# Optimization experiments

Measured on AMD Instinct MI355X. Metric: run time of the kernel, lower is better.

The kernel has to match this reference:

```python
import jax, jax.numpy as jnp
import numpy as np

SIGMA = 2.0


def _level(h, centers, W, b):
    # h: [n_prev, d], centers: [n_cur, d], W: [d, d] (torch Linear weight), b: [d]
    # squared distances via expansion: ||h||^2 - 2 h.c + ||c||^2  -> [n_prev, n_cur]
    sq = (jnp.sum(h * h, axis=1, keepdims=True)
          - 2.0 * (h @ centers.T)
          + jnp.sum(centers * centers, axis=1)[None, :])
    p = jax.nn.softmax(-sq / (2.0 * SIGMA), axis=1)  # softmax over centers per row
    t = jnp.tanh(h @ W.T + b)                        # [n_prev, d]
    # h_next[i] = sum_j p[j, i] * t[j]
    return p.T @ t                                   # [n_cur, d]


def setup_inputs() -> dict:
    key = jax.random.key(0)
    ks = jax.random.split(key, 11)
    d = 1024
    num_centers = [16384, 2048, 256, 32]
    inp = {"task_embedding": jax.random.normal(ks[0], (num_centers[0], d), dtype=jnp.float32)}
    # cluster centers per level (torch.rand -> uniform [0,1))
    inp["centers1"] = jax.random.uniform(ks[1], (num_centers[1], d), dtype=jnp.float32)
    inp["centers2"] = jax.random.uniform(ks[2], (num_centers[2], d), dtype=jnp.float32)
    inp["centers3"] = jax.random.uniform(ks[3], (num_centers[3], d), dtype=jnp.float32)
    # linear layers (Kaiming-uniform-ish init bound)
    bound = 1.0 / np.sqrt(d)
    for i, kw, kb in [(1, ks[4], ks[5]), (2, ks[6], ks[7]), (3, ks[8], ks[9])]:
        inp[f"W{i}"] = jax.random.uniform(kw, (d, d), minval=-bound, maxval=bound, dtype=jnp.float32)
        inp[f"b{i}"] = jax.random.uniform(kb, (d,), minval=-bound, maxval=bound, dtype=jnp.float32)
    return inp


def reference(task_embedding, centers1, centers2, centers3, W1, b1, W2, b2, W3, b3):
    h = task_embedding
    h = _level(h, centers1, W1, b1)
    h = _level(h, centers2, W2, b2)
    h = _level(h, centers3, W3, b3)
    return h
```

## Files before the change

kernel.cpp:

```cpp
#include <hip/hip_runtime.h>
#include <cmath>

typedef _Float16 half8 __attribute__((ext_vector_type(8)));
typedef _Float16 half4v __attribute__((ext_vector_type(4)));
typedef __attribute__((ext_vector_type(4))) float floatx4;

#define GLOAD_LDS16(gp, lp)                                            \
  __builtin_amdgcn_global_load_lds(                                    \
      (const __attribute__((address_space(1))) void*)(gp),             \
      (__attribute__((address_space(3))) void*)(lp), 16, 0, 0)

static inline int cdiv(int a, int b) { return (a + b - 1) / b; }

__global__ void prep(const float* __restrict__ h0, const float* __restrict__ W1,
                     const float* __restrict__ W2, const float* __restrict__ W3,
                     const float* __restrict__ c1, const float* __restrict__ c2,
                     const float* __restrict__ c3,
                     _Float16* __restrict__ hh, _Float16* __restrict__ Wh1,
                     _Float16* __restrict__ Wh2, _Float16* __restrict__ Wh3,
                     _Float16* __restrict__ cb1, _Float16* __restrict__ cb2,
                     _Float16* __restrict__ cb3,
                     float* __restrict__ cn1, float* __restrict__ cn2,
                     float* __restrict__ cn3,
                     int nh, int nw, int castBlocks, int n1, int n2) {
  int t = threadIdx.x;
  if ((int)blockIdx.x < castBlocks) {
    int gi = (blockIdx.x * 256 + t) * 4;
    const float* src; _Float16* dst; int off;
    if (gi < nh)                { src = h0; dst = hh;  off = gi; }
    else if (gi < nh + nw)      { src = W1; dst = Wh1; off = gi - nh; }
    else if (gi < nh + 2 * nw)  { src = W2; dst = Wh2; off = gi - nh - nw; }
    else if (gi < nh + 3 * nw)  { src = W3; dst = Wh3; off = gi - nh - 2 * nw; }
    else return;
    float4 v = *(const float4*)(src + off);
    half4v o = {(_Float16)v.x, (_Float16)v.y, (_Float16)v.z, (_Float16)v.w};
    *(half4v*)(dst + off) = o;
    return;
  }
  int row = blockIdx.x - castBlocks;
  const float* c; _Float16* cb; float* cn;
  if (row < n1)            { c = c1; cb = cb1; cn = cn1; }
  else if (row < n1 + n2)  { row -= n1; c = c2; cb = cb2; cn = cn2; }
  else                     { row -= n1 + n2; c = c3; cb = cb3; cn = cn3; }
  float4 v = *(const float4*)(c + (size_t)row * 1024 + t * 4);
  half4v o = {(_Float16)v.x, (_Float16)v.y, (_Float16)v.z, (_Float16)v.w};
  *(half4v*)(cb + (size_t)row * 1024 + t * 4) = o;
  float s = v.x * v.x + v.y * v.y + v.z * v.z + v.w * v.w;
  #pragma unroll
  for (int off = 32; off > 0; off >>= 1) s += __shfl_down(s, off, 64);
  __shared__ float ws[4];
  if ((t & 63) == 0) ws[t >> 6] = s;
  __syncthreads();
  if (t == 0) cn[row] = ws[0] + ws[1] + ws[2] + ws[3];
}

#define SM_CHUNK 64
__global__ void colexp_partial(_Float16* __restrict__ ST, const float* __restrict__ pmax,
                               float* __restrict__ psum, int mchunks, int ncur, int nprev) {
  int col = (blockIdx.x * 256 + threadIdx.x) * 4;
  if (col >= nprev) return;
  float m0 = -1e30f, m1 = -1e30f, m2 = -1e30f, m3 = -1e30f;
  for (int k = 0; k < mchunks; ++k) {
    float4 v = *(const float4*)(pmax + (size_t)k * nprev + col);
    m0 = fmaxf(m0, v.x); m1 = fmaxf(m1, v.y); m2 = fmaxf(m2, v.z); m3 = fmaxf(m3, v.w);
  }
  int j0 = blockIdx.y * SM_CHUNK;
  int j1 = min(j0 + SM_CHUNK, ncur);
  float s0 = 0.f, s1 = 0.f, s2 = 0.f, s3 = 0.f;
  for (int j = j0; j < j1; ++j) {
    size_t o = (size_t)j * nprev + col;
    half4v x = *(const half4v*)(ST + o);
    float e0 = __expf((float)x[0] - m0), e1 = __expf((float)x[1] - m1);
    float e2 = __expf((float)x[2] - m2), e3 = __expf((float)x[3] - m3);
    half4v e = {(_Float16)e0, (_Float16)e1, (_Float16)e2, (_Float16)e3};
    *(half4v*)(ST + o) = e;
    s0 += e0; s1 += e1; s2 += e2; s3 += e3;
  }
  float4 sv = {s0, s1, s2, s3};
  *(float4*)(psum + (size_t)blockIdx.y * nprev + col) = sv;
}

__global__ void reduce_parts(const _Float16* __restrict__ part, _Float16* __restrict__ out,
                             int mn, int S) {
  int i = (blockIdx.x * 256 + threadIdx.x) * 4;
  if (i >= mn) return;
  float a0 = 0.f, a1 = 0.f, a2 = 0.f, a3 = 0.f;
  for (int s = 0; s < S; ++s) {
    half4v v = *(const half4v*)(part + (size_t)s * mn + i);
    a0 += (float)v[0]; a1 += (float)v[1]; a2 += (float)v[2]; a3 += (float)v[3];
  }
  half4v o = {(_Float16)a0, (_Float16)a1, (_Float16)a2, (_Float16)a3};
  *(half4v*)(out + i) = o;
}

enum { EP_LOGIT = 0, EP_TANH = 1, EP_TANHP = 2, EP_F16 = 3, EP_F32 = 4, EP_PART = 5 };

template<int BM, int BN, int EPI>
__launch_bounds__(256, 4)
__global__ void gemm_nt(const _Float16* __restrict__ A,
                        const _Float16* __restrict__ B,
                        void* __restrict__ Cout,
                        const float* __restrict__ aux1,
                        const float* __restrict__ aux2,
                        float* __restrict__ pmax,
                        int pnchunks,
                        int M, int N, int K, int kLen) {
  constexpr int BK = 64;
  constexpr int WTM = BM / 2, WTN = BN / 2;
  constexpr int FM = WTM / 16, FN = WTN / 16;
  __shared__ __align__(16) _Float16 As[BM * BK];
  __shared__ __align__(16) _Float16 Bs[BN * BK];
  float* smf = (float*)As;
  const int tid  = threadIdx.x;
  const int lane = tid & 63;
  const int wave = tid >> 6;
  const int wm = wave >> 1, wn = wave & 1;
  const int mBase = blockIdx.x * BM, nBase = blockIdx.y * BN;
  const int kBase = blockIdx.z * kLen;
  const int lr    = lane & 15;
  const int kHalf = (lane >> 4) << 3;

  const int srOff  = lane >> 3;
  const int schunk = (lane & 7) ^ srOff;
  floatx4 acc[FM][FN] = {};
  constexpr int AV = BM * BK / (256 * 8);
  constexpr int BV = BN * BK / (256 * 8);

  for (int k0 = kBase; k0 < kBase + kLen; k0 += BK) {
    #pragma unroll
    for (int v = 0; v < AV; ++v) {
      int rowBase = v * 32 + wave * 8;
      int gm = mBase + rowBase + srOff;
      if (gm >= M) gm = M - 1;
      GLOAD_LDS16(A + (size_t)gm * K + k0 + schunk * 8, &As[rowBase * BK]);
    }
    #pragma unroll
    for (int v = 0; v < BV; ++v) {
      int rowBase = v * 32 + wave * 8;
      int gn = nBase + rowBase + srOff;
      if (gn >= N) gn = N - 1;
      GLOAD_LDS16(B + (size_t)gn * K + k0 + schunk * 8, &Bs[rowBase * BK]);
    }
    __syncthreads();
    #pragma unroll
    for (int kk = 0; kk < BK; kk += 32) {
      const int q = (kk + kHalf) >> 3;
      half8 af[FM], bfv[FN];
      #pragma unroll
      for (int i = 0; i < FM; ++i) {
        int r = wm * WTM + i * 16 + lr;
        af[i] = *(const half8*)(&As[r * BK + ((q ^ (r & 7)) << 3)]);
      }
      #pragma unroll
      for (int j = 0; j < FN; ++j) {
        int r = wn * WTN + j * 16 + lr;
        bfv[j] = *(const half8*)(&Bs[r * BK + ((q ^ (r & 7)) << 3)]);
      }
      #pragma unroll
      for (int i = 0; i < FM; ++i)
        #pragma unroll
        for (int j = 0; j < FN; ++j)
          acc[i][j] = __builtin_amdgcn_mfma_f32_16x16x32_f16(af[i], bfv[j], acc[i][j], 0, 0, 0);
    }
    __syncthreads();
  }

  if (EPI == EP_TANH) {
    if (tid < BN) {
      int col = nBase + tid;
      float ssum = 0.f;
      if (col < N)
        for (int k = 0; k < pnchunks; ++k) ssum += aux2[(size_t)k * N + col];
      smf[tid] = 1.f / ssum;
    }
    __syncthreads();
  }

  const int rBase = (lane >> 4) << 2;
  float lmax[FN];
  #pragma unroll
  for (int j = 0; j < FN; ++j) lmax[j] = -1e30f;
  #pragma unroll
  for (int i = 0; i < FM; ++i) {
    #pragma unroll
    for (int j = 0; j < FN; ++j) {
      #pragma unroll
      for (int r = 0; r < 4; ++r) {
        int row = mBase + wm * WTM + i * 16 + rBase + r;
        int col = nBase + wn * WTN + j * 16 + lr;
        if (row < M && col < N) {
          float v = acc[i][j][r];
          size_t o = (size_t)row * N + col;
          if (EPI == EP_LOGIT) {
            v = 0.5f * v - 0.25f * aux1[row];
            ((_Float16*)Cout)[o] = (_Float16)v;
            lmax[j] = fmaxf(lmax[j], v);
          } else if (EPI == EP_TANH) {
            v = tanhf(v + aux1[row]) * smf[col - nBase];
            ((_Float16*)Cout)[o] = (_Float16)v;
          } else if (EPI == EP_TANHP) {
            v = tanhf(v + aux1[row]);
            ((_Float16*)Cout)[o] = (_Float16)v;
          } else if (EPI == EP_F16) {
            ((_Float16*)Cout)[o] = (_Float16)v;
          } else if (EPI == EP_PART) {
            ((_Float16*)Cout)[(size_t)blockIdx.z * M * N + o] = (_Float16)v;
          } else {
            ((float*)Cout)[o] = v;
          }
        }
      }
    }
  }
  if (EPI == EP_LOGIT) {
    #pragma unroll
    for (int j = 0; j < FN; ++j) {
      float m = lmax[j];
      m = fmaxf(m, __shfl_xor(m, 16, 64));
      m = fmaxf(m, __shfl_xor(m, 32, 64));
      if ((lane >> 4) == 0) smf[wm * BN + wn * WTN + j * 16 + lr] = m;
    }
    __syncthreads();
    if (tid < BN) {
      int col = nBase + tid;
      if (col < N)
        pmax[(size_t)blockIdx.x * N + col] = fmaxf(smf[tid], smf[BN + tid]);
    }
  }
}

template<int BM, int BN>
__launch_bounds__(256, 2)
__global__ void fused_ls(const _Float16* __restrict__ A,
                         const _Float16* __restrict__ B,
                         _Float16* __restrict__ Eout,
                         const float* __restrict__ cn,
                         int M, int N, int K) {
  constexpr int BK = 64;
  constexpr int WTM = BM / 2, WTN = BN / 2;
  constexpr int FM = WTM / 16, FN = WTN / 16;
  constexpr int TLD = BN + 4;
  constexpr int STAGE_B = (BM + BN) * BK * 2;
  constexpr int TILE_B  = BM * TLD * 4;
  constexpr int SM_B = STAGE_B > TILE_B ? STAGE_B : TILE_B;
  __shared__ __align__(16) char smem[SM_B];
  _Float16* As = (_Float16*)smem;
  _Float16* Bs = As + BM * BK;
  float* tile = (float*)smem;
  __shared__ float redm[256], reds[256];
  const int tid  = threadIdx.x;
  const int lane = tid & 63;
  const int wave = tid >> 6;
  const int wm = wave >> 1, wn = wave & 1;
  const int nBase = blockIdx.x * BN;
  const int lr    = lane & 15;
  const int kHalf = (lane >> 4) << 3;
  const int srOff  = lane >> 3;
  const int schunk = (lane & 7) ^ srOff;
  floatx4 acc[FM][FN] = {};
  constexpr int AV = BM * BK / (256 * 8);
  constexpr int BV = BN * BK / (256 * 8);

  for (int k0 = 0; k0 < K; k0 += BK) {
    #pragma unroll
    for (int v = 0; v < AV; ++v) {
      int rowBase = v * 32 + wave * 8;
      GLOAD_LDS16(A + (size_t)(rowBase + srOff) * K + k0 + schunk * 8, &As[rowBase * BK]);
    }
    #pragma unroll
    for (int v = 0; v < BV; ++v) {
      int rowBase = v * 32 + wave * 8;
      GLOAD_LDS16(B + (size_t)(nBase + rowBase + srOff) * K + k0 + schunk * 8, &Bs[rowBase * BK]);
    }
    __syncthreads();
    #pragma unroll
    for (int kk = 0; kk < BK; kk += 32) {
      const int q = (kk + kHalf) >> 3;
      half8 af[FM], bfv[FN];
      #pragma unroll
      for (int i = 0; i < FM; ++i) {
        int r = wm * WTM + i * 16 + lr;
        af[i] = *(const half8*)(&As[r * BK + ((q ^ (r & 7)) << 3)]);
      }
      #pragma unroll
      for (int j = 0; j < FN; ++j) {
        int r = wn * WTN + j * 16 + lr;
        bfv[j] = *(const half8*)(&Bs[r * BK + ((q ^ (r & 7)) << 3)]);
      }
      #pragma unroll
      for (int i = 0; i < FM; ++i)
        #pragma unroll
        for (int j = 0; j < FN; ++j)
          acc[i][j] = __builtin_amdgcn_mfma_f32_16x16x32_f16(af[i], bfv[j], acc[i][j], 0, 0, 0);
    }
    __syncthreads();
  }

  const int rBase = (lane >> 4) << 2;
  #pragma unroll
  for (int i = 0; i < FM; ++i)
    #pragma unroll
    for (int j = 0; j < FN; ++j)
      #pragma unroll
      for (int r = 0; r < 4; ++r) {
        int row = wm * WTM + i * 16 + rBase + r;
        int col = wn * WTN + j * 16 + lr;
        tile[row * TLD + col] = 0.5f * acc[i][j][r] - 0.25f * cn[row];
      }
  __syncthreads();

  constexpr int P = 256 / BN;
  const int c = tid & (BN - 1);
  const int p = tid / BN;
  float m = -1e30f;
  for (int j = p; j < M; j += P) m = fmaxf(m, tile[j * TLD + c]);
  redm[p * BN + c] = m;
  __syncthreads();
  float mf = redm[c];
  #pragma unroll
  for (int q = 1; q < P; ++q) mf = fmaxf(mf, redm[q * BN + c]);
  float s = 0.f;
  for (int j = p; j < M; j += P) {
    float e = __expf(tile[j * TLD + c] - mf);
    tile[j * TLD + c] = e;
    s += e;
  }
  reds[p * BN + c] = s;
  __syncthreads();
  float l = 0.f;
  #pragma unroll
  for (int q = 0; q < P; ++q) l += reds[q * BN + c];
  const float li = 1.f / l;
  for (int j = p; j < M; j += P)
    Eout[(size_t)j * N + nBase + c] = (_Float16)(tile[j * TLD + c] * li);
}

template<int EPI>
static int launch_gemm(int M, int N, int K, const _Float16* A, const _Float16* B,
                       void* C, const float* a1, const float* a2, float* pmax,
                       int pnchunks, hipStream_t s) {
  long b128   = (long)cdiv(M, 128) * cdiv(N, 128);
  long b12864 = (long)cdiv(M, 128) * cdiv(N, 64);
  if (b128 >= 192) {
    gemm_nt<128, 128, EPI><<<dim3(cdiv(M, 128), cdiv(N, 128)), 256, 0, s>>>(
        A, B, C, a1, a2, pmax, pnchunks, M, N, K, K);
    return 128;
  } else if (M >= 128 && b12864 >= 192) {
    gemm_nt<128, 64, EPI><<<dim3(cdiv(M, 128), cdiv(N, 64)), 256, 0, s>>>(
        A, B, C, a1, a2, pmax, pnchunks, M, N, K, K);
    return 128;
  } else {
    gemm_nt<64, 64, EPI><<<dim3(cdiv(M, 64), cdiv(N, 64)), 256, 0, s>>>(
        A, B, C, a1, a2, pmax, pnchunks, M, N, K, K);
    return 64;
  }
}

static void launch_gemm_splitk(int M, int N, int K, int S,
                               const _Float16* A, const _Float16* B,
                               _Float16* Cpart, _Float16* Cout, hipStream_t s) {
  int kLen = K / S;
  long b128 = (long)cdiv(M, 128) * cdiv(N, 128) * S;
  if (M >= 128 && N >= 128 && b128 >= 256) {
    gemm_nt<128, 128, EP_PART><<<dim3(cdiv(M, 128), cdiv(N, 128), S), 256, 0, s>>>(
        A, B, Cpart, nullptr, nullptr, nullptr, 0, M, N, K, kLen);
  } else {
    gemm_nt<64, 64, EP_PART><<<dim3(cdiv(M, 64), cdiv(N, 64), S), 256, 0, s>>>(
        A, B, Cpart, nullptr, nullptr, nullptr, 0, M, N, K, kLen);
  }
  int mn = M * N;
  reduce_parts<<<cdiv(mn, 1024), 256, 0, s>>>(Cpart, Cout, mn, S);
}

extern "C" void kernel_launch(void* const* d_in, const int* in_sizes, int n_in,
                              void* d_out, int out_size, void* d_ws, size_t ws_size,
                              hipStream_t stream) {
  const float* h0 = (const float*)d_in[0];
  const float* c1 = (const float*)d_in[1];
  const float* c2 = (const float*)d_in[2];
  const float* c3 = (const float*)d_in[3];
  const float* W1 = (const float*)d_in[4];
  const float* b1 = (const float*)d_in[5];
  const float* W2 = (const float*)d_in[6];
  const float* b2 = (const float*)d_in[7];
  const float* W3 = (const float*)d_in[8];
  const float* b3 = (const float*)d_in[9];

  const int d = 1024;
  const int N0 = 16384, N1 = 2048, N2 = 256, N3 = 32;

  char* w = (char*)d_ws;
  size_t off = 0;
  auto alloc = [&](size_t bytes) {
    void* p = w + off;
    off += (bytes + 255) & ~(size_t)255;
    return p;
  };
  _Float16* hb  = (_Float16*)alloc((size_t)N0 * d * 2);
  _Float16* cb1 = (_Float16*)alloc((size_t)N1 * d * 2);
  _Float16* cb2 = (_Float16*)alloc((size_t)N2 * d * 2);
  _Float16* cb3 = (_Float16*)alloc((size_t)N3 * d * 2);
  float* cn1 = (float*)alloc((size_t)N1 * 4);
  float* cn2 = (float*)alloc((size_t)N2 * 4);
  float* cn3 = (float*)alloc((size_t)N3 * 4);
  _Float16* Wb1 = (_Float16*)alloc((size_t)d * d * 2);
  _Float16* Wb2 = (_Float16*)alloc((size_t)d * d * 2);
  _Float16* Wb3 = (_Float16*)alloc((size_t)d * d * 2);
  _Float16* ST = (_Float16*)alloc((size_t)N1 * N0 * 2);
  _Float16* tT = (_Float16*)alloc((size_t)d * N0 * 2);
  float* pmax = (float*)alloc((size_t)32 * N0 * 4);
  float* psum = (float*)alloc((size_t)32 * N0 * 4);
  _Float16* h1b = (_Float16*)alloc((size_t)N1 * d * 2);
  _Float16* h2b = (_Float16*)alloc((size_t)N2 * d * 2);
  _Float16* Cpart = (_Float16*)alloc((size_t)8 * N1 * d * 2);
  _Float16* E = ST;
  (void)ws_size; (void)in_sizes; (void)n_in; (void)out_size;

  int nh = N0 * d, nw = d * d;
  int castBlocks = cdiv(nh + 3 * nw, 1024);
  prep<<<castBlocks + N1 + N2 + N3, 256, 0, stream>>>(
      h0, W1, W2, W3, c1, c2, c3, hb, Wb1, Wb2, Wb3, cb1, cb2, cb3,
      cn1, cn2, cn3, nh, nw, castBlocks, N1, N2);

  int bm = launch_gemm<EP_LOGIT>(N1, N0, d, cb1, hb, ST, cn1, nullptr, pmax, 0, stream);
  colexp_partial<<<dim3(N0 / 1024, cdiv(N1, SM_CHUNK)), 256, 0, stream>>>(
      ST, pmax, psum, cdiv(N1, bm), N1, N0);
  launch_gemm<EP_TANH>(d, N0, d, Wb1, hb, tT, b1, psum, nullptr, cdiv(N1, SM_CHUNK), stream);
  launch_gemm_splitk(N1, d, N0, 8, E, tT, Cpart, h1b, stream);

  fused_ls<256, 64><<<N1 / 64, 256, 0, stream>>>(cb2, h1b, E, cn2, N2, N1, d);
  launch_gemm<EP_TANHP>(d, N1, d, Wb2, h1b, tT, b2, nullptr, nullptr, 0, stream);
  launch_gemm_splitk(N2, d, N1, 8, E, tT, Cpart, h2b, stream);

  fused_ls<32, 64><<<N2 / 64, 256, 0, stream>>>(cb3, h2b, E, cn3, N3, N2, d);
  launch_gemm<EP_TANHP>(d, N2, d, Wb3, h2b, tT, b3, nullptr, nullptr, 0, stream);
  launch_gemm<EP_F32>(N3, d, N2, E, tT, d_out, nullptr, nullptr, nullptr, 0, stream);
}
```

Before: 483.4 us.

## Add 256x256 8-wave pipelined MFMA GEMM for level-1 large GEMMs

```diff
diff --git a/kernel.cpp b/kernel.cpp
--- a/kernel.cpp
+++ b/kernel.cpp
@@ -227,6 +227,212 @@
         pmax[(size_t)blockIdx.x * N + col] = fmaxf(smf[tid], smf[BN + tid]);
     }
   }
+}
+
+#define BAR8 __builtin_amdgcn_s_barrier()
+#define LGKM0 asm volatile("s_waitcnt lgkmcnt(0)" ::: "memory")
+#define VMC(n) asm volatile("s_waitcnt vmcnt(" #n ")" ::: "memory")
+#define STG_A(b, kk, h)                                                              \
+  do {                                                                               \
+    GLOAD_LDS16(gA + (size_t)((h) * 128) * K + (kk),                                 \
+                &As[b][((h) * 128 + wave * 8) * 64]);                                \
+    GLOAD_LDS16(gA + (size_t)((h) * 128 + 64) * K + (kk),                            \
+                &As[b][((h) * 128 + 64 + wave * 8) * 64]);                           \
+  } while (0)
+#define STG_B(b, kk, h)                                                              \
+  do {                                                                               \
+    GLOAD_LDS16(gB + (size_t)((h) * 128) * K + (kk),                                 \
+                &Bs[b][((h) * 128 + wave * 8) * 64]);                                \
+    GLOAD_LDS16(gB + (size_t)((h) * 128 + 64) * K + (kk),                            \
+                &Bs[b][((h) * 128 + 64 + wave * 8) * 64]);                           \
+  } while (0)
+#define LDA8(s, base)                                                                \
+  { _Pragma("unroll") for (int i_ = 0; i_ < 8; ++i_)                                 \
+      af[s][i_] = *(const half8*)((base) + aoff + i_ * 1024 + ((s) ? xr1 : xr0)); }
+#define LDB2(s, j0, base)                                                            \
+  { bf[s][(j0)] = *(const half8*)((base) + boff + (j0) * 1024 + ((s) ? xr1 : xr0));  \
+    bf[s][(j0) + 1] =                                                                \
+        *(const half8*)((base) + boff + ((j0) + 1) * 1024 + ((s) ? xr1 : xr0)); }
+#define MF16(s, nh)                                                                  \
+  { __builtin_amdgcn_s_setprio(1);                                                   \
+    _Pragma("unroll") for (int i_ = 0; i_ < 8; ++i_) {                               \
+      acc[i_][2 * (nh)] = __builtin_amdgcn_mfma_f32_16x16x32_f16(                    \
+          af[s][i_], bf[s][2 * (nh)], acc[i_][2 * (nh)], 0, 0, 0);                   \
+      acc[i_][2 * (nh) + 1] = __builtin_amdgcn_mfma_f32_16x16x32_f16(                \
+          af[s][i_], bf[s][2 * (nh) + 1], acc[i_][2 * (nh) + 1], 0, 0, 0);           \
+    }                                                                                \
+    __builtin_amdgcn_s_setprio(0); }
+
+template<int EPI>
+__launch_bounds__(512, 2)
+__global__ void gemm8(const _Float16* __restrict__ A, const _Float16* __restrict__ B,
+                      void* __restrict__ Cout, const float* __restrict__ aux1,
+                      const float* __restrict__ aux2, float* __restrict__ pmax,
+                      int pnchunks, int M, int N, int K, int kLen) {
+  __shared__ __align__(16) _Float16 As[2][256 * 64];
+  __shared__ __align__(16) _Float16 Bs[2][256 * 64];
+  float* smf = (float*)&As[0][0];
+  const int tid  = threadIdx.x;
+  const int lane = tid & 63;
+  const int wave = tid >> 6;
+  const int wm = wave >> 2, wn = wave & 3;
+  const int mBase = blockIdx.x * 256, nBase = blockIdx.y * 256;
+  const int kBase = blockIdx.z * kLen;
+  const int lr = lane & 15;
+  const int xr0 = (((lane >> 4) ^ (lr & 7)) << 3);
+  const int xr1 = ((((lane >> 4) + 4) ^ (lr & 7)) << 3);
+  const int aoff = (wm * 128 + lr) * 64;
+  const int boff = (wn * 64 + lr) * 64;
+  const int srOff = lane >> 3;
+  const int sch8 = ((lane & 7) ^ srOff) << 3;
+  const _Float16* gA = A + (size_t)(mBase + wave * 8 + srOff) * K + kBase + sch8;
+  const _Float16* gB = B + (size_t)(nBase + wave * 8 + srOff) * K + kBase + sch8;
+  const _Float16* As0 = &As[0][0];
+  const _Float16* As1 = &As[1][0];
+  const _Float16* Bs0 = &Bs[0][0];
+  const _Float16* Bs1 = &Bs[1][0];
+
+  half8 af[2][8], bf[2][4];
+  floatx4 acc[8][4] = {};
+  const int NT = kLen / 64;
+
+  STG_A(0, 0, 0); STG_A(0, 0, 1); STG_B(0, 0, 0); STG_B(0, 0, 1);
+  STG_A(1, 64, 0); STG_A(1, 64, 1); STG_B(1, 64, 0);
+  VMC(6);
+  BAR8;
+  LDA8(0, As0);
+  LDB2(0, 0, Bs0);
+
+  int kc = 0;
+  for (int t = 0; t + 3 < NT; t += 2, kc += 128) {
+    LDB2(0, 2, Bs0);  STG_B(1, kc + 64, 1);
+    BAR8; LGKM0; MF16(0, 0); BAR8;
+    LDA8(1, As0);  LDB2(1, 0, Bs0);
+    BAR8; LGKM0; MF16(0, 1); BAR8;
+    LDB2(1, 2, Bs0);  STG_A(0, kc + 128, 0);  VMC(2);
+    BAR8; LGKM0; MF16(1, 0); BAR8;
+    LDA8(0, As1);  LDB2(0, 0, Bs1);  STG_A(0, kc + 128, 1);  STG_B(0, kc + 128, 0);
+    BAR8; LGKM0; MF16(1, 1); BAR8;
+    LDB2(0, 2, Bs1);  STG_B(0, kc + 128, 1);
+    BAR8; LGKM0; MF16(0, 0); BAR8;
+    LDA8(1, As1);  LDB2(1, 0, Bs1);
+    BAR8; LGKM0; MF16(0, 1); BAR8;
+    LDB2(1, 2, Bs1);  STG_A(1, kc + 192, 0);  VMC(2);
+    BAR8; LGKM0; MF16(1, 0); BAR8;
+    LDA8(0, As0);  LDB2(0, 0, Bs0);  STG_A(1, kc + 192, 1);  STG_B(1, kc + 192, 0);
+    BAR8; LGKM0; MF16(1, 1); BAR8;
+  }
+  LDB2(0, 2, Bs0);  STG_B(1, kc + 64, 1);
+  BAR8; LGKM0; MF16(0, 0); BAR8;
+  LDA8(1, As0);  LDB2(1, 0, Bs0);
+  BAR8; LGKM0; MF16(0, 1); BAR8;
+  LDB2(1, 2, Bs0);  VMC(0);
+  BAR8; LGKM0; MF16(1, 0); BAR8;
+  LDA8(0, As1);  LDB2(0, 0, Bs1);
+  BAR8; LGKM0; MF16(1, 1); BAR8;
+  LDB2(0, 2, Bs1);
+  BAR8; LGKM0; MF16(0, 0); BAR8;
+  LDA8(1, As1);  LDB2(1, 0, Bs1);
+  BAR8; LGKM0; MF16(0, 1); BAR8;
+  LDB2(1, 2, Bs1);
+  BAR8; LGKM0; MF16(1, 0); BAR8;
+  MF16(1, 1);
+  __syncthreads();
+
+  if (EPI == EP_TANH) {
+    if (tid < 256) {
+      int col = nBase + tid;
+      float ssum = 0.f;
+      for (int k = 0; k < pnchunks; ++k) ssum += aux2[(size_t)k * N + col];
+      smf[tid] = 1.f / ssum;
+    }
+    __syncthreads();
+  }
+
+  const int rBase = (lane >> 4) << 2;
+  float lmax[4];
+  #pragma unroll
+  for (int j = 0; j < 4; ++j) lmax[j] = -1e30f;
+  #pragma unroll
+  for (int i = 0; i < 8; ++i)
+    #pragma unroll
+    for (int j = 0; j < 4; ++j)
+      #pragma unroll
+      for (int r = 0; r < 4; ++r) {
+        int row = mBase + wm * 128 + i * 16 + rBase + r;
+        int col = nBase + wn * 64 + j * 16 + lr;
+        float v = acc[i][j][r];
+        size_t o = (size_t)row * N + col;
+        if (EPI == EP_LOGIT) {
+          v = 0.5f * v - 0.25f * aux1[row];
+          ((_Float16*)Cout)[o] = (_Float16)v;
+          lmax[j] = fmaxf(lmax[j], v);
+        } else if (EPI == EP_TANH) {
+          v = tanhf(v + aux1[row]) * smf[col - nBase];
+          ((_Float16*)Cout)[o] = (_Float16)v;
+        } else {
+          ((_Float16*)Cout)[(size_t)blockIdx.z * M * N + o] = (_Float16)v;
+        }
+      }
+  if (EPI == EP_LOGIT) {
+    #pragma unroll
+    for (int j = 0; j < 4; ++j) {
+      float m2 = lmax[j];
+      m2 = fmaxf(m2, __shfl_xor(m2, 16, 64));
+      m2 = fmaxf(m2, __shfl_xor(m2, 32, 64));
+      if ((lane >> 4) == 0) smf[wm * 256 + wn * 64 + j * 16 + lr] = m2;
+    }
+    __syncthreads();
+    if (tid < 256) {
+      int col = nBase + tid;
+      pmax[(size_t)blockIdx.x * N + col] = fmaxf(smf[tid], smf[256 + tid]);
+    }
+  }
+}
+#undef BAR8
+#undef LGKM0
+#undef VMC
+#undef STG_A
+#undef STG_B
+#undef LDA8
+#undef LDB2
+#undef MF16
+
+template<int EPI>
+static int launch_gemm(int M, int N, int K, const _Float16* A, const _Float16* B,
+                       void* C, const float* a1, const float* a2, float* pmax,
+                       int pnchunks, hipStream_t s) {
+  long b128   = (long)cdiv(M, 128) * cdiv(N, 128);
+  long b12864 = (long)cdiv(M, 128) * cdiv(N, 64);
+  if (b128 >= 192) {
+    gemm_nt<128, 128, EPI><<<dim3(cdiv(M, 128), cdiv(N, 128)), 256, 0, s>>>(
+        A, B, C, a1, a2, pmax, pnchunks, M, N, K, K);
+    return 128;
+  } else if (M >= 128 && b12864 >= 192) {
+    gemm_nt<128, 64, EPI><<<dim3(cdiv(M, 128), cdiv(N, 64)), 256, 0, s>>>(
+        A, B, C, a1, a2, pmax, pnchunks, M, N, K, K);
+    return 128;
+  } else {
+    gemm_nt<64, 64, EPI><<<dim3(cdiv(M, 64), cdiv(N, 64)), 256, 0, s>>>(
+        A, B, C, a1, a2, pmax, pnchunks, M, N, K, K);
+    return 64;
+  }
+}
+
+static void launch_gemm_splitk(int M, int N, int K, int S,
+                               const _Float16* A, const _Float16* B,
+                               _Float16* Cpart, _Float16* Cout, hipStream_t s) {
+  int kLen = K / S;
+  long b128 = (long)cdiv(M, 128) * cdiv(N, 128) * S;
+  if (M >= 128 && N >= 128 && b128 >= 256) {
+    gemm_nt<128, 128, EP_PART><<<dim3(cdiv(M, 128), cdiv(N, 128), S), 256, 0, s>>>(
+        A, B, Cpart, nullptr, nullptr, nullptr, 0, M, N, K, kLen);
+  } else {
+    gemm_nt<64, 64, EP_PART><<<dim3(cdiv(M, 64), cdiv(N, 64), S), 256, 0, s>>>(
+        A, B, Cpart, nullptr, nullptr, nullptr, 0, M, N, K, kLen);
+  }
+  int mn = M * N;
+  reduce_parts<<<cdiv(mn, 1024), 256, 0, s>>>(Cpart, Cout, mn, S);
 }
 
 template<int BM, int BN>
@@ -335,43 +541,6 @@
     Eout[(size_t)j * N + nBase + c] = (_Float16)(tile[j * TLD + c] * li);
 }
 
-template<int EPI>
-static int launch_gemm(int M, int N, int K, const _Float16* A, const _Float16* B,
-                       void* C, const float* a1, const float* a2, float* pmax,
-                       int pnchunks, hipStream_t s) {
-  long b128   = (long)cdiv(M, 128) * cdiv(N, 128);
-  long b12864 = (long)cdiv(M, 128) * cdiv(N, 64);
-  if (b128 >= 192) {
-    gemm_nt<128, 128, EPI><<<dim3(cdiv(M, 128), cdiv(N, 128)), 256, 0, s>>>(
-        A, B, C, a1, a2, pmax, pnchunks, M, N, K, K);
-    return 128;
-  } else if (M >= 128 && b12864 >= 192) {
-    gemm_nt<128, 64, EPI><<<dim3(cdiv(M, 128), cdiv(N, 64)), 256, 0, s>>>(
-        A, B, C, a1, a2, pmax, pnchunks, M, N, K, K);
-    return 128;
-  } else {
-    gemm_nt<64, 64, EPI><<<dim3(cdiv(M, 64), cdiv(N, 64)), 256, 0, s>>>(
-        A, B, C, a1, a2, pmax, pnchunks, M, N, K, K);
-    return 64;
-  }
-}
-
-static void launch_gemm_splitk(int M, int N, int K, int S,
-                               const _Float16* A, const _Float16* B,
-                               _Float16* Cpart, _Float16* Cout, hipStream_t s) {
-  int kLen = K / S;
-  long b128 = (long)cdiv(M, 128) * cdiv(N, 128) * S;
-  if (M >= 128 && N >= 128 && b128 >= 256) {
-    gemm_nt<128, 128, EP_PART><<<dim3(cdiv(M, 128), cdiv(N, 128), S), 256, 0, s>>>(
-        A, B, Cpart, nullptr, nullptr, nullptr, 0, M, N, K, kLen);
-  } else {
-    gemm_nt<64, 64, EP_PART><<<dim3(cdiv(M, 64), cdiv(N, 64), S), 256, 0, s>>>(
-        A, B, Cpart, nullptr, nullptr, nullptr, 0, M, N, K, kLen);
-  }
-  int mn = M * N;
-  reduce_parts<<<cdiv(mn, 1024), 256, 0, s>>>(Cpart, Cout, mn, S);
-}
-
 extern "C" void kernel_launch(void* const* d_in, const int* in_sizes, int n_in,
                               void* d_out, int out_size, void* d_ws, size_t ws_size,
                               hipStream_t stream) {
@@ -422,11 +591,15 @@
       h0, W1, W2, W3, c1, c2, c3, hb, Wb1, Wb2, Wb3, cb1, cb2, cb3,
       cn1, cn2, cn3, nh, nw, castBlocks, N1, N2);
 
-  int bm = launch_gemm<EP_LOGIT>(N1, N0, d, cb1, hb, ST, cn1, nullptr, pmax, 0, stream);
+  gemm8<EP_LOGIT><<<dim3(N1 / 256, N0 / 256), 512, 0, stream>>>(
+      cb1, hb, ST, cn1, nullptr, pmax, 0, N1, N0, d, d);
   colexp_partial<<<dim3(N0 / 1024, cdiv(N1, SM_CHUNK)), 256, 0, stream>>>(
-      ST, pmax, psum, cdiv(N1, bm), N1, N0);
-  launch_gemm<EP_TANH>(d, N0, d, Wb1, hb, tT, b1, psum, nullptr, cdiv(N1, SM_CHUNK), stream);
-  launch_gemm_splitk(N1, d, N0, 8, E, tT, Cpart, h1b, stream);
+      ST, pmax, psum, N1 / 256, N1, N0);
+  gemm8<EP_TANH><<<dim3(d / 256, N0 / 256), 512, 0, stream>>>(
+      Wb1, hb, tT, b1, psum, nullptr, cdiv(N1, SM_CHUNK), d, N0, d, d);
+  gemm8<EP_PART><<<dim3(N1 / 256, d / 256, 8), 512, 0, stream>>>(
+      E, tT, Cpart, nullptr, nullptr, nullptr, 0, N1, d, N0, N0 / 8);
+  reduce_parts<<<cdiv(N1 * d, 1024), 256, 0, stream>>>(Cpart, h1b, N1 * d, 8);
 
   fused_ls<256, 64><<<N1 / 64, 256, 0, stream>>>(cb2, h1b, E, cn2, N2, N1, d);
   launch_gemm<EP_TANHP>(d, N1, d, Wb2, h1b, tT, b2, nullptr, nullptr, 0, stream);
```

After: 522.9 us. 8.2% more time.

## Fuse split-K reduction into GEMM and merge independent level kernels

Applied to the files above, without the earlier changes.

```diff
diff --git a/kernel.cpp b/kernel.cpp
--- a/kernel.cpp
+++ b/kernel.cpp
@@ -11,6 +11,7 @@
       (__attribute__((address_space(3))) void*)(lp), 16, 0, 0)
 
 static inline int cdiv(int a, int b) { return (a + b - 1) / b; }
+
 
 __global__ void prep(const float* __restrict__ h0, const float* __restrict__ W1,
                      const float* __restrict__ W2, const float* __restrict__ W3,
@@ -80,43 +81,30 @@
   *(float4*)(psum + (size_t)blockIdx.y * nprev + col) = sv;
 }
 
-__global__ void reduce_parts(const _Float16* __restrict__ part, _Float16* __restrict__ out,
-                             int mn, int S) {
-  int i = (blockIdx.x * 256 + threadIdx.x) * 4;
-  if (i >= mn) return;
-  float a0 = 0.f, a1 = 0.f, a2 = 0.f, a3 = 0.f;
-  for (int s = 0; s < S; ++s) {
-    half4v v = *(const half4v*)(part + (size_t)s * mn + i);
-    a0 += (float)v[0]; a1 += (float)v[1]; a2 += (float)v[2]; a3 += (float)v[3];
-  }
-  half4v o = {(_Float16)a0, (_Float16)a1, (_Float16)a2, (_Float16)a3};
-  *(half4v*)(out + i) = o;
-}
-
 enum { EP_LOGIT = 0, EP_TANH = 1, EP_TANHP = 2, EP_F16 = 3, EP_F32 = 4, EP_PART = 5 };
 
 template<int BM, int BN, int EPI>
-__launch_bounds__(256, 4)
-__global__ void gemm_nt(const _Float16* __restrict__ A,
-                        const _Float16* __restrict__ B,
-                        void* __restrict__ Cout,
-                        const float* __restrict__ aux1,
-                        const float* __restrict__ aux2,
-                        float* __restrict__ pmax,
-                        int pnchunks,
-                        int M, int N, int K, int kLen) {
+__device__ __forceinline__ void gemm_body(
+    const _Float16* __restrict__ A, const _Float16* __restrict__ B,
+    void* __restrict__ Cout,
+    const float* __restrict__ aux1,
+    const float* __restrict__ aux2,
+    float* __restrict__ pmax,
+    int pnchunks,
+    int M, int N, int K, int kLen,
+    int bx, int by, int bz,
+    int* __restrict__ cnt, _Float16* __restrict__ fout, int S, int nTilesY,
+    _Float16* As, _Float16* Bs) {
   constexpr int BK = 64;
   constexpr int WTM = BM / 2, WTN = BN / 2;
   constexpr int FM = WTM / 16, FN = WTN / 16;
-  __shared__ __align__(16) _Float16 As[BM * BK];
-  __shared__ __align__(16) _Float16 Bs[BN * BK];
   float* smf = (float*)As;
   const int tid  = threadIdx.x;
   const int lane = tid & 63;
   const int wave = tid >> 6;
   const int wm = wave >> 1, wn = wave & 1;
-  const int mBase = blockIdx.x * BM, nBase = blockIdx.y * BN;
-  const int kBase = blockIdx.z * kLen;
+  const int mBase = bx * BM, nBase = by * BN;
+  const int kBase = bz * kLen;
   const int lr    = lane & 15;
   const int kHalf = (lane >> 4) << 3;
 
@@ -204,7 +192,7 @@
           } else if (EPI == EP_F16) {
             ((_Float16*)Cout)[o] = (_Float16)v;
           } else if (EPI == EP_PART) {
-            ((_Float16*)Cout)[(size_t)blockIdx.z * M * N + o] = (_Float16)v;
+            ((_Float16*)Cout)[(size_t)bz * M * N + o] = (_Float16)v;
           } else {
             ((float*)Cout)[o] = v;
           }
@@ -224,35 +212,75 @@
     if (tid < BN) {
       int col = nBase + tid;
       if (col < N)
-        pmax[(size_t)blockIdx.x * N + col] = fmaxf(smf[tid], smf[BN + tid]);
-    }
-  }
+        pmax[(size_t)bx * N + col] = fmaxf(smf[tid], smf[BN + tid]);
+    }
+  }
+  if (EPI == EP_PART) {
+    if (cnt != nullptr) {
+      __shared__ int lastFlag;
+      __threadfence();
+      __syncthreads();
+      if (tid == 0) {
+        int old = atomicAdd(&cnt[bx * nTilesY + by], 1);
+        lastFlag = (old == S - 1) ? 1 : 0;
+      }
+      __syncthreads();
+      if (lastFlag) {
+        __threadfence();
+        const int mn = M * N;
+        const _Float16* part = (const _Float16*)Cout;
+        for (int e = tid * 4; e < BM * BN; e += 1024) {
+          int rr = e / BN, cc = e % BN;
+          int row = mBase + rr, col = nBase + cc;
+          if (row < M && col < N) {
+            float a0 = 0.f, a1 = 0.f, a2 = 0.f, a3 = 0.f;
+            size_t o = (size_t)row * N + col;
+            for (int s = 0; s < S; ++s) {
+              half4v v = *(const half4v*)(part + (size_t)s * mn + o);
+              a0 += (float)v[0]; a1 += (float)v[1]; a2 += (float)v[2]; a3 += (float)v[3];
+            }
+            half4v ov = {(_Float16)a0, (_Float16)a1, (_Float16)a2, (_Float16)a3};
+            *(half4v*)(fout + o) = ov;
+          }
+        }
+      }
+    }
+  }
+}
+
+template<int BM, int BN, int EPI>
+__launch_bounds__(256, 4)
+__global__ void gemm_nt(const _Float16* __restrict__ A, const _Float16* __restrict__ B,
+                        void* __restrict__ Cout, const float* __restrict__ aux1,
+                        const float* __restrict__ aux2, float* __restrict__ pmax,
+                        int pnchunks, int M, int N, int K, int kLen,
+                        int* cnt, _Float16* fout, int S) {
+  __shared__ __align__(16) _Float16 As[BM * 64];
+  __shared__ __align__(16) _Float16 Bs[BN * 64];
+  gemm_body<BM, BN, EPI>(A, B, Cout, aux1, aux2, pmax, pnchunks, M, N, K, kLen,
+                         blockIdx.x, blockIdx.y, blockIdx.z,
+                         cnt, fout, S, gridDim.y, As, Bs);
 }
 
 template<int BM, int BN>
-__launch_bounds__(256, 2)
-__global__ void fused_ls(const _Float16* __restrict__ A,
-                         const _Float16* __restrict__ B,
-                         _Float16* __restrict__ Eout,
-                         const float* __restrict__ cn,
-                         int M, int N, int K) {
+__device__ __forceinline__ void fused_ls_body(
+    const _Float16* __restrict__ A,
+    const _Float16* __restrict__ B,
+    _Float16* __restrict__ Eout,
+    const float* __restrict__ cn,
+    int M, int N, int K, int nBase,
+    char* smem, float* redm, float* reds) {
   constexpr int BK = 64;
   constexpr int WTM = BM / 2, WTN = BN / 2;
   constexpr int FM = WTM / 16, FN = WTN / 16;
   constexpr int TLD = BN + 4;
-  constexpr int STAGE_B = (BM + BN) * BK * 2;
-  constexpr int TILE_B  = BM * TLD * 4;
-  constexpr int SM_B = STAGE_B > TILE_B ? STAGE_B : TILE_B;
-  __shared__ __align__(16) char smem[SM_B];
   _Float16* As = (_Float16*)smem;
   _Float16* Bs = As + BM * BK;
   float* tile = (float*)smem;
-  __shared__ float redm[256], reds[256];
   const int tid  = threadIdx.x;
   const int lane = tid & 63;
   const int wave = tid >> 6;
   const int wm = wave >> 1, wn = wave & 1;
-  const int nBase = blockIdx.x * BN;
   const int lr    = lane & 15;
   const int kHalf = (lane >> 4) << 3;
   const int srOff  = lane >> 3;
@@ -335,41 +363,46 @@
     Eout[(size_t)j * N + nBase + c] = (_Float16)(tile[j * TLD + c] * li);
 }
 
-template<int EPI>
-static int launch_gemm(int M, int N, int K, const _Float16* A, const _Float16* B,
-                       void* C, const float* a1, const float* a2, float* pmax,
-                       int pnchunks, hipStream_t s) {
-  long b128   = (long)cdiv(M, 128) * cdiv(N, 128);
-  long b12864 = (long)cdiv(M, 128) * cdiv(N, 64);
-  if (b128 >= 192) {
-    gemm_nt<128, 128, EPI><<<dim3(cdiv(M, 128), cdiv(N, 128)), 256, 0, s>>>(
-        A, B, C, a1, a2, pmax, pnchunks, M, N, K, K);
-    return 128;
-  } else if (M >= 128 && b12864 >= 192) {
-    gemm_nt<128, 64, EPI><<<dim3(cdiv(M, 128), cdiv(N, 64)), 256, 0, s>>>(
-        A, B, C, a1, a2, pmax, pnchunks, M, N, K, K);
-    return 128;
+__launch_bounds__(256, 1)
+__global__ void lvl2_merged(const _Float16* __restrict__ cb2,
+                            const _Float16* __restrict__ h1b,
+                            _Float16* __restrict__ E, const float* __restrict__ cn2,
+                            const _Float16* __restrict__ Wb2,
+                            _Float16* __restrict__ tT, const float* __restrict__ b2) {
+  __shared__ __align__(16) char smemF[36864];
+  __shared__ float redm[256], reds[256];
+  __shared__ __align__(16) _Float16 AsG[128 * 64];
+  __shared__ __align__(16) _Float16 BsG[64 * 64];
+  if ((int)blockIdx.x < 64) {
+    fused_ls_body<256, 32>(cb2, h1b, E, cn2, 256, 2048, 1024, blockIdx.x * 32,
+                           smemF, redm, reds);
   } else {
-    gemm_nt<64, 64, EPI><<<dim3(cdiv(M, 64), cdiv(N, 64)), 256, 0, s>>>(
-        A, B, C, a1, a2, pmax, pnchunks, M, N, K, K);
-    return 64;
-  }
-}
-
-static void launch_gemm_splitk(int M, int N, int K, int S,
-                               const _Float16* A, const _Float16* B,
-                               _Float16* Cpart, _Float16* Cout, hipStream_t s) {
-  int kLen = K / S;
-  long b128 = (long)cdiv(M, 128) * cdiv(N, 128) * S;
-  if (M >= 128 && N >= 128 && b128 >= 256) {
-    gemm_nt<128, 128, EP_PART><<<dim3(cdiv(M, 128), cdiv(N, 128), S), 256, 0, s>>>(
-        A, B, Cpart, nullptr, nullptr, nullptr, 0, M, N, K, kLen);
+    int lin = blockIdx.x - 64;
+    gemm_body<128, 64, EP_TANHP>(Wb2, h1b, tT, b2, nullptr, nullptr, 0,
+                                 1024, 2048, 1024, 1024, lin % 8, lin / 8, 0,
+                                 nullptr, nullptr, 0, 0, AsG, BsG);
+  }
+}
+
+__launch_bounds__(256, 2)
+__global__ void lvl3_merged(const _Float16* __restrict__ cb3,
+                            const _Float16* __restrict__ h2b,
+                            _Float16* __restrict__ E, const float* __restrict__ cn3,
+                            const _Float16* __restrict__ Wb3,
+                            _Float16* __restrict__ tT, const float* __restrict__ b3) {
+  __shared__ __align__(16) char smemF[12288];
+  __shared__ float redm[256], reds[256];
+  __shared__ __align__(16) _Float16 AsG[64 * 64];
+  __shared__ __align__(16) _Float16 BsG[64 * 64];
+  if ((int)blockIdx.x < 4) {
+    fused_ls_body<32, 64>(cb3, h2b, E, cn3, 32, 256, 1024, blockIdx.x * 64,
+                          smemF, redm, reds);
   } else {
-    gemm_nt<64, 64, EP_PART><<<dim3(cdiv(M, 64), cdiv(N, 64), S), 256, 0, s>>>(
-        A, B, Cpart, nullptr, nullptr, nullptr, 0, M, N, K, kLen);
-  }
-  int mn = M * N;
-  reduce_parts<<<cdiv(mn, 1024), 256, 0, s>>>(Cpart, Cout, mn, S);
+    int lin = blockIdx.x - 4;
+    gemm_body<64, 64, EP_TANHP>(Wb3, h2b, tT, b3, nullptr, nullptr, 0,
+                                1024, 256, 1024, 1024, lin % 16, lin / 16, 0,
+                                nullptr, nullptr, 0, 0, AsG, BsG);
+  }
 }
 
 extern "C" void kernel_launch(void* const* d_in, const int* in_sizes, int n_in,
@@ -413,8 +446,12 @@
   _Float16* h1b = (_Float16*)alloc((size_t)N1 * d * 2);
   _Float16* h2b = (_Float16*)alloc((size_t)N2 * d * 2);
   _Float16* Cpart = (_Float16*)alloc((size_t)8 * N1 * d * 2);
+  int* cnt1 = (int*)alloc(128 * 4);
+  int* cnt2 = (int*)alloc(64 * 4);
   _Float16* E = ST;
-  (void)ws_size; (void)in_sizes; (void)n_in; (void)out_size;
+  (void)ws_size; (void)in_sizes; (void)n_in; (void)out_size; (void)cnt2;
+
+  hipMemsetAsync(cnt1, 0, 192 * 4, stream);
 
   int nh = N0 * d, nw = d * d;
   int castBlocks = cdiv(nh + 3 * nw, 1024);
@@ -422,17 +459,24 @@
       h0, W1, W2, W3, c1, c2, c3, hb, Wb1, Wb2, Wb3, cb1, cb2, cb3,
       cn1, cn2, cn3, nh, nw, castBlocks, N1, N2);
 
-  int bm = launch_gemm<EP_LOGIT>(N1, N0, d, cb1, hb, ST, cn1, nullptr, pmax, 0, stream);
+  gemm_nt<128, 128, EP_LOGIT><<<dim3(16, 128), 256, 0, stream>>>(
+      cb1, hb, ST, cn1, nullptr, pmax, 0, N1, N0, d, d, nullptr, nullptr, 0);
   colexp_partial<<<dim3(N0 / 1024, cdiv(N1, SM_CHUNK)), 256, 0, stream>>>(
-      ST, pmax, psum, cdiv(N1, bm), N1, N0);
-  launch_gemm<EP_TANH>(d, N0, d, Wb1, hb, tT, b1, psum, nullptr, cdiv(N1, SM_CHUNK), stream);
-  launch_gemm_splitk(N1, d, N0, 8, E, tT, Cpart, h1b, stream);
-
-  fused_ls<256, 64><<<N1 / 64, 256, 0, stream>>>(cb2, h1b, E, cn2, N2, N1, d);
-  launch_gemm<EP_TANHP>(d, N1, d, Wb2, h1b, tT, b2, nullptr, nullptr, 0, stream);
-  launch_gemm_splitk(N2, d, N1, 8, E, tT, Cpart, h2b, stream);
-
-  fused_ls<32, 64><<<N2 / 64, 256, 0, stream>>>(cb3, h2b, E, cn3, N3, N2, d);
-  launch_gemm<EP_TANHP>(d, N2, d, Wb3, h2b, tT, b3, nullptr, nullptr, 0, stream);
-  launch_gemm<EP_F32>(N3, d, N2, E, tT, d_out, nullptr, nullptr, nullptr, 0, stream);
-}
+      ST, pmax, psum, 16, N1, N0);
+  gemm_nt<128, 128, EP_TANH><<<dim3(8, 128), 256, 0, stream>>>(
+      Wb1, hb, tT, b1, psum, nullptr, cdiv(N1, SM_CHUNK), d, N0, d, d,
+      nullptr, nullptr, 0);
+  gemm_nt<128, 128, EP_PART><<<dim3(16, 8, 8), 256, 0, stream>>>(
+      E, tT, Cpart, nullptr, nullptr, nullptr, 0, N1, d, N0, N0 / 8,
+      cnt1, h1b, 8);
+
+  lvl2_merged<<<64 + 256, 256, 0, stream>>>(cb2, h1b, E, cn2, Wb2, tT, b2);
+  gemm_nt<64, 64, EP_PART><<<dim3(4, 16, 8), 256, 0, stream>>>(
+      E, tT, Cpart, nullptr, nullptr, nullptr, 0, N2, d, N1, N1 / 8,
+      cnt2, h2b, 8);
+
+  lvl3_merged<<<4 + 64, 256, 0, stream>>>(cb3, h2b, E, cn3, Wb3, tT, b3);
+  gemm_nt<64, 64, EP_F32><<<dim3(1, 16), 256, 0, stream>>>(
+      E, tT, d_out, nullptr, nullptr, nullptr, 0, N3, d, N2, N2,
+      nullptr, nullptr, 0);
+}
```

After: 723.0 us. 49.6% more time.
